# Kernel tuning notes

Hardware: AMD Instinct MI355X
Metric: run time of the kernel (lower is better)

The kernel has to match this reference:

```python
import jax, jax.numpy as jnp
import numpy as np

B, T, C = 4, 2048, 1024
N_HEADS = 16
HEAD_DIM = C // N_HEADS


def setup_inputs() -> dict:
    key = jax.random.key(0)
    k1, k2, k3, k4, k5 = jax.random.split(key, 5)
    x = jax.random.normal(k1, (B, T, C), dtype=jnp.float32)
    # torch Linear: y = x @ W.T + b; store W as [out, in]
    w_qkv = jax.random.normal(k2, (3 * C, C), dtype=jnp.float32) * (1.0 / np.sqrt(C))
    b_qkv = jax.random.normal(k3, (3 * C,), dtype=jnp.float32) * 0.01
    w_proj = jax.random.normal(k4, (C, C), dtype=jnp.float32) * (1.0 / np.sqrt(C))
    b_proj = jax.random.normal(k5, (C,), dtype=jnp.float32) * 0.01
    return {"x": x, "w_qkv": w_qkv, "b_qkv": b_qkv, "w_proj": w_proj, "b_proj": b_proj}


def reference(x, w_qkv, b_qkv, w_proj, b_proj):
    Bx, Tx, Cx = x.shape
    scale = 1.0 / np.sqrt(HEAD_DIM)
    qkv = x @ w_qkv.T + b_qkv                              # [B,T,3C]
    qkv = qkv.reshape(Bx, Tx, 3, N_HEADS, HEAD_DIM)
    qkv = jnp.transpose(qkv, (2, 0, 3, 1, 4))              # [3,B,H,T,D]
    q, k, v = qkv[0], qkv[1], qkv[2]
    att = jnp.einsum('bhqd,bhkd->bhqk', q, k) * scale      # [B,H,T,T]
    causal = jnp.tril(jnp.ones((Tx, Tx), dtype=bool))
    att = jnp.where(causal[None, None, :, :], att, -jnp.inf)
    att = jax.nn.softmax(att, axis=-1)
    # dropout p=0.0 (eval) -> identity
    out = jnp.einsum('bhqk,bhkd->bhqd', att, v)            # [B,H,T,D]
    out = jnp.transpose(out, (0, 2, 1, 3)).reshape(Bx, Tx, Cx)
    return out @ w_proj.T + b_proj
```

## Files before the change

### kernel.cpp

```cpp
#include <hip/hip_runtime.h>
#include <hip/hip_bf16.h>
#include <cstdint>

typedef __attribute__((ext_vector_type(8))) short bf16x8;
typedef __attribute__((ext_vector_type(4))) float f32x4;
typedef __attribute__((ext_vector_type(16))) float f32x16;

#define MFMA16(a, b, c) __builtin_amdgcn_mfma_f32_16x16x32_bf16(a, b, c, 0, 0, 0)
#define MFMA32(a, b, c) __builtin_amdgcn_mfma_f32_32x32x16_bf16(a, b, c, 0, 0, 0)

typedef __attribute__((address_space(1))) uint32_t as1_u32;
typedef __attribute__((address_space(3))) uint32_t as3_u32;
static __device__ __forceinline__ void gload16(const void* g, void* l) {
  __builtin_amdgcn_global_load_lds((as1_u32*)g, (as3_u32*)l, 16, 0, 0);
}

static __device__ __forceinline__ ushort f2b(float f) {
  union { float f; uint32_t u; } v; v.f = f;
  uint32_t u = v.u;
  uint32_t r = (u + 0x7FFFu + ((u >> 16) & 1u)) >> 16;
  return (ushort)r;
}

static __device__ __forceinline__ uint32_t cvtpk(float a, float b) {
  uint32_t r;
  asm("v_cvt_pk_bf16_f32 %0, %1, %2" : "=v"(r) : "v"(a), "v"(b));
  return r;
}
static __device__ __forceinline__ void plswap(uint32_t& a, uint32_t& b) {
  asm volatile("v_permlane32_swap_b32 %0, %1" : "+v"(a), "+v"(b));
}

#define QSCALE 0.1803368782f

#define LOFF(r, kc4) (((r) >> 1) * 64 + ((((((r) & 1) << 2) | (kc4)) ^ (((r) >> 1) & 7)) * 8))

#define N4_X  2097152
#define N4_WQ 786432
#define N4_WP 262144
__global__ void cvt_all(const float* __restrict__ x, const float* __restrict__ wq,
                        const float* __restrict__ wp, ushort* __restrict__ xb,
                        ushort* __restrict__ wqb, ushort* __restrict__ wpb) {
  int i = blockIdx.x * blockDim.x + threadIdx.x;
  const float* src; ushort* dst; int j;
  if (i < N4_X)            { src = x;  dst = xb;  j = i; }
  else if (i < N4_X + N4_WQ) { src = wq; dst = wqb; j = i - N4_X; }
  else                     { src = wp; dst = wpb; j = i - (N4_X + N4_WQ); }
  const float4 v = ((const float4*)src)[j];
  ushort4 o;
  o.x = f2b(v.x); o.y = f2b(v.y); o.z = f2b(v.z); o.w = f2b(v.w);
  ((ushort4*)dst)[j] = o;
}

__global__ __launch_bounds__(512, 2) void gemm_qkv256(
    const ushort* __restrict__ A,
    const ushort* __restrict__ W,
    const float* __restrict__ bias,
    int K, int nbx, int nbase,
    ushort* __restrict__ q_ws, ushort* __restrict__ k_ws, ushort* __restrict__ v_ws) {
  __shared__ ushort As[2][2][2][64 * 64];
  __shared__ ushort Bs[2][2][2][64 * 64];
  const int tid = threadIdx.x;
  const int cpx = gridDim.x >> 3;
  const int wg = (blockIdx.x & 7) * cpx + (blockIdx.x >> 3);
  const int m0 = (wg / nbx) * 256, n0 = nbase + (wg % nbx) * 256;
  const int wid = tid >> 6, lane = tid & 63;
  const int wr = wid >> 2, wc = wid & 3;
  const int lr = lane & 15, lg = lane >> 4;
  const int bhalf = wc >> 1, brow = (wc & 1) * 64;
  const int prow = tid >> 3, pchk = tid & 7;
  const int lchk = pchk ^ (prow & 7);
  const int srow = prow * 2 + (lchk >> 2);
  const int skc = (lchk & 3) * 8;

  f32x4 acc[8][4] = {};
  const int nt = K >> 6;

#define STA(db_, half_, kt_)                                                  \
  { const ushort* src = A + (size_t)(m0 + (half_)*128 + srow) * K + (kt_)*64 + skc; \
    gload16(src, &As[db_][half_][0][tid * 8]);                                \
    gload16(src + 32, &As[db_][half_][1][tid * 8]); }
#define STB(db_, half_, kt_)                                                  \
  { const ushort* src = W + (size_t)(n0 + (half_)*128 + srow) * K + (kt_)*64 + skc; \
    gload16(src, &Bs[db_][half_][0][tid * 8]);                                \
    gload16(src + 32, &Bs[db_][half_][1][tid * 8]); }

  STB(0, 0, 0); STB(0, 1, 0);
  STA(0, 0, 0); STA(0, 1, 0);
  STB(1, 0, 1); STB(1, 1, 1);
  asm volatile("s_waitcnt vmcnt(4)" ::: "memory");
  __builtin_amdgcn_s_barrier();

  for (int T = 0; T < nt; ++T) {
    const int db = T & 1;
    const ushort* Ak0 = &As[db][wr][0][0];
    const ushort* Ak1 = &As[db][wr][1][0];
    const ushort* Bk0 = &Bs[db][bhalf][0][0];
    const ushort* Bk1 = &Bs[db][bhalf][1][0];
    bf16x8 b[4][2];
    {
      bf16x8 a[4][2];
#pragma unroll
      for (int mm = 0; mm < 4; ++mm) {
        const int r = mm * 16 + lr;
        a[mm][0] = *(const bf16x8*)&Ak0[LOFF(r, lg)];
        a[mm][1] = *(const bf16x8*)&Ak1[LOFF(r, lg)];
      }
#pragma unroll
      for (int nf = 0; nf < 4; ++nf) {
        const int rr = brow + nf * 16 + lr;
        b[nf][0] = *(const bf16x8*)&Bk0[LOFF(rr, lg)];
        b[nf][1] = *(const bf16x8*)&Bk1[LOFF(rr, lg)];
      }
      if (T + 1 < nt) { STA(db ^ 1, 0, T + 1); STA(db ^ 1, 1, T + 1); }
      __builtin_amdgcn_sched_barrier(0);
      __builtin_amdgcn_s_barrier();
      asm volatile("s_waitcnt lgkmcnt(0)" ::: "memory");
      __builtin_amdgcn_sched_barrier(0);
      __builtin_amdgcn_s_setprio(1);
#pragma unroll
      for (int kk = 0; kk < 2; ++kk)
#pragma unroll
        for (int mm = 0; mm < 4; ++mm)
#pragma unroll
          for (int nf = 0; nf < 4; ++nf)
            acc[mm][nf] = MFMA16(a[mm][kk], b[nf][kk], acc[mm][nf]);
      __builtin_amdgcn_s_setprio(0);
      __builtin_amdgcn_s_barrier();
    }
    {
      bf16x8 a[4][2];
#pragma unroll
      for (int mm = 0; mm < 4; ++mm) {
        const int r = (4 + mm) * 16 + lr;
        a[mm][0] = *(const bf16x8*)&Ak0[LOFF(r, lg)];
        a[mm][1] = *(const bf16x8*)&Ak1[LOFF(r, lg)];
      }
      if (T + 2 < nt) { STB(db, 0, T + 2); STB(db, 1, T + 2); }
      __builtin_amdgcn_sched_barrier(0);
      __builtin_amdgcn_s_barrier();
      asm volatile("s_waitcnt lgkmcnt(0)" ::: "memory");
      __builtin_amdgcn_sched_barrier(0);
      __builtin_amdgcn_s_setprio(1);
#pragma unroll
      for (int kk = 0; kk < 2; ++kk)
#pragma unroll
        for (int mm = 0; mm < 4; ++mm)
#pragma unroll
          for (int nf = 0; nf < 4; ++nf)
            acc[4 + mm][nf] = MFMA16(a[mm][kk], b[nf][kk], acc[4 + mm][nf]);
      __builtin_amdgcn_s_setprio(0);
      if (T + 2 < nt)
        asm volatile("s_waitcnt vmcnt(4)" ::: "memory");
      else if (T + 1 < nt)
        asm volatile("s_waitcnt vmcnt(0)" ::: "memory");
      if (T + 1 < nt) __builtin_amdgcn_s_barrier();
    }
  }
#undef STA
#undef STB

#pragma unroll
  for (int mf = 0; mf < 8; ++mf) {
#pragma unroll
    for (int nf = 0; nf < 4; ++nf) {
      const int rowb = m0 + wr * 128 + mf * 16 + lg * 4;
      const int col = n0 + wc * 64 + nf * 16 + lr;
      float v[4];
#pragma unroll
      for (int i = 0; i < 4; ++i) v[i] = acc[mf][nf][i] + bias[col];
      const int sel = col >> 10;
      const int rem = col & 1023;
      const int h = rem >> 6, d = rem & 63;
      const int bb = rowb >> 11, t0 = rowb & 2047;
      if (sel == 2) {
        ushort4 st;
        st.x = f2b(v[0]); st.y = f2b(v[1]); st.z = f2b(v[2]); st.w = f2b(v[3]);
        *(ushort4*)&v_ws[((size_t)(bb * 16 + h) * 64 + d) * 2048 + t0] = st;
      } else if (sel == 0) {
#pragma unroll
        for (int i = 0; i < 4; ++i)
          q_ws[((size_t)(bb * 16 + h) * 2048 + t0 + i) * 64 + d] = f2b(v[i] * QSCALE);
      } else {
#pragma unroll
        for (int i = 0; i < 4; ++i)
          k_ws[((size_t)(bb * 16 + h) * 2048 + t0 + i) * 64 + d] = f2b(v[i]);
      }
    }
  }
}

template<int EPI>
__global__ __launch_bounds__(512, 2) void gemm_2ph(
    const ushort* __restrict__ A,
    const ushort* __restrict__ W,
    const float* __restrict__ bias,
    int K, int Nout, int nbx, int nbase,
    ushort* __restrict__ q_ws, ushort* __restrict__ k_ws, ushort* __restrict__ v_ws,
    float* __restrict__ out) {
  __shared__ ushort As[2][2][64 * 64];
  __shared__ ushort Bs[2][2][2][64 * 64];
  const int tid = threadIdx.x;
  const int cpx = gridDim.x >> 3;
  const int wg = (blockIdx.x & 7) * cpx + (blockIdx.x >> 3);
  const int m0 = (wg / nbx) * 128, n0 = nbase + (wg % nbx) * 256;
  const int wid = tid >> 6, lane = tid & 63;
  const int wr = wid >> 2, wc = wid & 3;
  const int lr = lane & 15, lg = lane >> 4;
  const int prow = tid >> 3, pchk = tid & 7;
  const int lchk = pchk ^ (prow & 7);
  const int srow = prow * 2 + (lchk >> 2);
  const int skc = (lchk & 3) * 8;

  f32x4 acc[4][4] = {};
  const int nt = K >> 6;

#define STA(db_, kt_)                                                         \
  { const ushort* src = A + (size_t)(m0 + srow) * K + (kt_)*64 + skc;         \
    gload16(src, &As[db_][0][tid * 8]);                                       \
    gload16(src + 32, &As[db_][1][tid * 8]); }
#define STB(db_, half_, kt_)                                                  \
  { const ushort* src = W + (size_t)(n0 + (half_)*128 + srow) * K + (kt_)*64 + skc; \
    gload16(src, &Bs[db_][half_][0][tid * 8]);                                \
    gload16(src + 32, &Bs[db_][half_][1][tid * 8]); }

  STB(0, 0, 0); STB(0, 1, 0);
  STA(0, 0);
  STB(1, 0, 1); STB(1, 1, 1);
  asm volatile("s_waitcnt vmcnt(4)" ::: "memory");
  __builtin_amdgcn_s_barrier();

  const int bhalf = wc >> 1, brow = (wc & 1) * 64;
  for (int T = 0; T < nt; ++T) {
    const int db = T & 1;
    const ushort* Asub0 = &As[db][0][0];
    const ushort* Asub1 = &As[db][1][0];
    const ushort* Bsub0 = &Bs[db][bhalf][0][0];
    const ushort* Bsub1 = &Bs[db][bhalf][1][0];
    bf16x8 b[4][2];
    {
      bf16x8 a[2][2];
#pragma unroll
      for (int mm = 0; mm < 2; ++mm) {
        const int r = wr * 64 + mm * 16 + lr;
        a[mm][0] = *(const bf16x8*)&Asub0[LOFF(r, lg)];
        a[mm][1] = *(const bf16x8*)&Asub1[LOFF(r, lg)];
      }
#pragma unroll
      for (int nf = 0; nf < 4; ++nf) {
        const int r = brow + nf * 16 + lr;
        b[nf][0] = *(const bf16x8*)&Bsub0[LOFF(r, lg)];
        b[nf][1] = *(const bf16x8*)&Bsub1[LOFF(r, lg)];
      }
      if (T + 1 < nt) STA((T + 1) & 1, T + 1);
      __builtin_amdgcn_sched_barrier(0);
      __builtin_amdgcn_s_barrier();
      asm volatile("s_waitcnt lgkmcnt(0)" ::: "memory");
      __builtin_amdgcn_sched_barrier(0);
      __builtin_amdgcn_s_setprio(1);
#pragma unroll
      for (int kk = 0; kk < 2; ++kk)
#pragma unroll
        for (int mm = 0; mm < 2; ++mm)
#pragma unroll
          for (int nf = 0; nf < 4; ++nf)
            acc[mm][nf] = MFMA16(a[mm][kk], b[nf][kk], acc[mm][nf]);
      __builtin_amdgcn_s_setprio(0);
      __builtin_amdgcn_s_barrier();
    }
    {
      bf16x8 a[2][2];
#pragma unroll
      for (int mm = 0; mm < 2; ++mm) {
        const int r = wr * 64 + (2 + mm) * 16 + lr;
        a[mm][0] = *(const bf16x8*)&Asub0[LOFF(r, lg)];
        a[mm][1] = *(const bf16x8*)&Asub1[LOFF(r, lg)];
      }
      if (T + 2 < nt) { STB(db, 0, T + 2); STB(db, 1, T + 2); }
      __builtin_amdgcn_sched_barrier(0);
      __builtin_amdgcn_s_barrier();
      asm volatile("s_waitcnt lgkmcnt(0)" ::: "memory");
      __builtin_amdgcn_sched_barrier(0);
      __builtin_amdgcn_s_setprio(1);
#pragma unroll
      for (int kk = 0; kk < 2; ++kk)
#pragma unroll
        for (int mm = 0; mm < 2; ++mm)
#pragma unroll
          for (int nf = 0; nf < 4; ++nf)
            acc[2 + mm][nf] = MFMA16(a[mm][kk], b[nf][kk], acc[2 + mm][nf]);
      __builtin_amdgcn_s_setprio(0);
      if (T + 2 < nt)
        asm volatile("s_waitcnt vmcnt(4)" ::: "memory");
      else if (T + 1 < nt)
        asm volatile("s_waitcnt vmcnt(0)" ::: "memory");
      if (T + 1 < nt) __builtin_amdgcn_s_barrier();
    }
  }
#undef STA
#undef STB

#pragma unroll
  for (int mf = 0; mf < 4; ++mf) {
#pragma unroll
    for (int nf = 0; nf < 4; ++nf) {
      const int rowb = m0 + wr * 64 + mf * 16 + lg * 4;
      const int col = n0 + wc * 64 + nf * 16 + lr;
      float v[4];
#pragma unroll
      for (int i = 0; i < 4; ++i) v[i] = acc[mf][nf][i] + bias[col];
      if (EPI == 0) {
        const int sel = col >> 10;
        const int rem = col & 1023;
        const int h = rem >> 6, d = rem & 63;
        const int bb = rowb >> 11, t0 = rowb & 2047;
        if (sel == 2) {
          ushort4 st;
          st.x = f2b(v[0]); st.y = f2b(v[1]); st.z = f2b(v[2]); st.w = f2b(v[3]);
          *(ushort4*)&v_ws[((size_t)(bb * 16 + h) * 64 + d) * 2048 + t0] = st;
        } else if (sel == 0) {
#pragma unroll
          for (int i = 0; i < 4; ++i)
            q_ws[((size_t)(bb * 16 + h) * 2048 + t0 + i) * 64 + d] = f2b(v[i] * QSCALE);
        } else {
#pragma unroll
          for (int i = 0; i < 4; ++i)
            k_ws[((size_t)(bb * 16 + h) * 2048 + t0 + i) * 64 + d] = f2b(v[i]);
        }
      } else {
#pragma unroll
        for (int i = 0; i < 4; ++i)
          out[(size_t)(rowb + i) * Nout + col] = v[i];
      }
    }
  }
}

__global__ __launch_bounds__(256, 4) void attn_v6(
    const ushort* __restrict__ Q, const ushort* __restrict__ K,
    const ushort* __restrict__ VT, ushort* __restrict__ O ) {
  const int blk = blockIdx.x;
  const int s = 15 - (blk >> 6);
  const int bh = blk & 63;
  const int tid = threadIdx.x;
  const int w = tid >> 6, lane = tid & 63;
  const int l31 = lane & 31, l5 = lane >> 5;
  const int bb = bh >> 4, h = bh & 15;
  const size_t base = (size_t)bh * 2048 * 64;
  const ushort* Qb = Q + base;
  const ushort* Kb = K + base;
  const ushort* VTb = VT + base;

  __shared__ ushort Ks[2][64 * 64];
  __shared__ ushort Vs[2][64 * 64];
  __shared__ float l_lds[4][32];

#define STAGE(buf, kt_)                                              \
  do {                                                               \
    const ushort* Kt = Kb + (size_t)(kt_) * 64 * 64;                 \
    const ushort* Vt = VTb + (kt_) * 64;                             \
    _Pragma("unroll") for (int i_ = 0; i_ < 2; ++i_) {               \
      const int ch = i_ * 256 + tid;                                 \
      const int r = ch >> 3;                                         \
      const int csw = ((ch & 7) ^ (r & 7)) * 8;                      \
      gload16(&Kt[(size_t)r * 64 + csw], &Ks[buf][ch * 8]);          \
      gload16(&Vt[(size_t)r * 2048 + csw], &Vs[buf][ch * 8]);        \
    }                                                                \
  } while (0)

  const int q0w = s * 128 + w * 32;
  const int nt = 2 * s + 2;
  const int qlane = q0w + l31;

  bf16x8 qf[4];
#pragma unroll
  for (int dblk = 0; dblk < 4; ++dblk)
    qf[dblk] = *(const bf16x8*)&Qb[(size_t)qlane * 64 + dblk * 16 + l5 * 8];

  f32x16 o0 = {}, o1 = {};
  float lsum = 0.f;

  STAGE(0, 0);
  __syncthreads();

  for (int kt = 0; kt < nt; ++kt) {
    const int cur = kt & 1;
    if (kt + 1 < nt) STAGE(cur ^ 1, kt + 1);
    const int k0 = kt << 6;
    const ushort* Ksc = Ks[cur];
    const ushort* Vsc = Vs[cur];
#pragma unroll
    for (int kblk = 0; kblk < 2; ++kblk) {
      const int kbase = k0 + kblk * 32;
      if (kbase <= q0w + 31) {
        f32x16 st = {};
        __builtin_amdgcn_s_setprio(1);
#pragma unroll
        for (int dblk = 0; dblk < 4; ++dblk) {
          const int row = kblk * 32 + l31;
          bf16x8 ka = *(const bf16x8*)&Ksc[row * 64 + (((dblk * 2 + l5) ^ (row & 7)) * 8)];
          st = MFMA32(ka, qf[dblk], st);
        }
        __builtin_amdgcn_s_setprio(0);
        if (kbase + 31 > q0w) {
#pragma unroll
          for (int r = 0; r < 16; ++r) {
            const int kk = kbase + (r & 3) + 8 * (r >> 2) + 4 * l5;
            st[r] = (kk <= qlane) ? st[r] : -INFINITY;
          }
        }
        float p[16];
#pragma unroll
        for (int r = 0; r < 16; ++r) {
          p[r] = __builtin_amdgcn_exp2f(st[r]);
          lsum += p[r];
        }
#pragma unroll
        for (int sbl = 0; sbl < 2; ++sbl) {
          uint32_t P0 = cvtpk(p[8 * sbl + 0], p[8 * sbl + 1]);
          uint32_t P1 = cvtpk(p[8 * sbl + 2], p[8 * sbl + 3]);
          uint32_t P2 = cvtpk(p[8 * sbl + 4], p[8 * sbl + 5]);
          uint32_t P3 = cvtpk(p[8 * sbl + 6], p[8 * sbl + 7]);
          plswap(P0, P2);
          plswap(P1, P3);
          union { uint32_t u[4]; bf16x8 v; } pk;
          pk.u[0] = P0; pk.u[1] = P1; pk.u[2] = P2; pk.u[3] = P3;
          const int kchunk = kblk * 4 + sbl * 2 + l5;
          __builtin_amdgcn_s_setprio(1);
#pragma unroll
          for (int db2 = 0; db2 < 2; ++db2) {
            const int vrow = db2 * 32 + l31;
            bf16x8 vb = *(const bf16x8*)&Vsc[vrow * 64 + ((kchunk ^ (vrow & 7)) * 8)];
            if (db2 == 0) o0 = MFMA32(pk.v, vb, o0);
            else          o1 = MFMA32(pk.v, vb, o1);
          }
          __builtin_amdgcn_s_setprio(0);
        }
      }
    }
    __syncthreads();
  }

  const float lfull = lsum + __shfl_xor(lsum, 32);
  if (lane < 32) l_lds[w][lane] = 1.f / lfull;
#pragma unroll
  for (int r = 0; r < 16; ++r) {
    const int qoff = (r & 3) + 8 * (r >> 2) + 4 * l5;
    const float inv = l_lds[w][qoff];
    const int t = q0w + qoff;
    ushort* op = &O[(size_t)(bb * 2048 + t) * 1024 + h * 64 + l31];
    op[0] = f2b(o0[r] * inv);
    op[32] = f2b(o1[r] * inv);
  }
#undef STAGE
}

extern "C" void kernel_launch(void* const* d_in, const int* in_sizes, int n_in,
                              void* d_out, int out_size, void* d_ws, size_t ws_size,
                              hipStream_t stream) {
  const float* x = (const float*)d_in[0];
  const float* w_qkv = (const float*)d_in[1];
  const float* b_qkv = (const float*)d_in[2];
  const float* w_proj = (const float*)d_in[3];
  const float* b_proj = (const float*)d_in[4];
  float* out = (float*)d_out;

  char* ws = (char*)d_ws;
  const size_t SZ_X = (size_t)8192 * 1024 * 2;
  const size_t SZ_WQ = (size_t)3072 * 1024 * 2;
  const size_t SZ_WP = (size_t)1024 * 1024 * 2;
  ushort* xb = (ushort*)(ws);
  ushort* wqb = (ushort*)(ws + SZ_X);
  ushort* wpb = (ushort*)(ws + SZ_X + SZ_WQ);
  ushort* q_ws = (ushort*)(ws + SZ_X + SZ_WQ + SZ_WP);
  ushort* k_ws = q_ws + (size_t)8192 * 1024;
  ushort* v_ws = k_ws + (size_t)8192 * 1024;

  cvt_all<<<(N4_X + N4_WQ + N4_WP) / 256, 256, 0, stream>>>(
      x, w_qkv, w_proj, xb, wqb, wpb);

  gemm_qkv256<<<256, 512, 0, stream>>>(
      xb, wqb, b_qkv, 1024, 8, 0, q_ws, k_ws, v_ws);

  gemm_2ph<0><<<256, 512, 0, stream>>>(
      xb, wqb, b_qkv, 1024, 0, 4, 2048, q_ws, k_ws, v_ws, nullptr);

  attn_v6<<<1024, 256, 0, stream>>>(q_ws, k_ws, v_ws, xb);

  gemm_2ph<1><<<256, 512, 0, stream>>>(
      xb, wpb, b_proj, 1024, 1024, 4, 0, nullptr, nullptr, nullptr, out);
}
```

Before: 153.0 us.

## Pipeline attention K/V staging with vmcnt waits and MFMA-based row sums

```diff
diff --git a/kernel.cpp b/kernel.cpp
--- a/kernel.cpp
+++ b/kernel.cpp
@@ -336,7 +336,7 @@
   }
 }
 
-__global__ __launch_bounds__(256, 4) void attn_v6(
+__global__ __launch_bounds__(256, 4) void attn_v7(
     const ushort* __restrict__ Q, const ushort* __restrict__ K,
     const ushort* __restrict__ VT, ushort* __restrict__ O ) {
   const int blk = blockIdx.x;
@@ -353,7 +353,6 @@
 
   __shared__ ushort Ks[2][64 * 64];
   __shared__ ushort Vs[2][64 * 64];
-  __shared__ float l_lds[4][32];
 
 #define STAGE(buf, kt_)                                              \
   do {                                                               \
@@ -372,81 +371,90 @@
   const int nt = 2 * s + 2;
   const int qlane = q0w + l31;
 
+  const int r7 = l31 & 7;
+  int offs[4];
+#pragma unroll
+  for (int i = 0; i < 4; ++i) offs[i] = l31 * 64 + (((2 * i + l5) ^ r7) << 3);
+
   bf16x8 qf[4];
 #pragma unroll
   for (int dblk = 0; dblk < 4; ++dblk)
     qf[dblk] = *(const bf16x8*)&Qb[(size_t)qlane * 64 + dblk * 16 + l5 * 8];
 
-  f32x16 o0 = {}, o1 = {};
-  float lsum = 0.f;
+  const bf16x8 vone = {0x3F80, 0x3F80, 0x3F80, 0x3F80, 0x3F80, 0x3F80, 0x3F80, 0x3F80};
+
+  f32x16 o0 = {}, o1 = {}, lacc = {};
 
   STAGE(0, 0);
-  __syncthreads();
-
-  for (int kt = 0; kt < nt; ++kt) {
-    const int cur = kt & 1;
-    if (kt + 1 < nt) STAGE(cur ^ 1, kt + 1);
-    const int k0 = kt << 6;
-    const ushort* Ksc = Ks[cur];
-    const ushort* Vsc = Vs[cur];
-#pragma unroll
-    for (int kblk = 0; kblk < 2; ++kblk) {
-      const int kbase = k0 + kblk * 32;
-      if (kbase <= q0w + 31) {
-        f32x16 st = {};
-        __builtin_amdgcn_s_setprio(1);
-#pragma unroll
-        for (int dblk = 0; dblk < 4; ++dblk) {
-          const int row = kblk * 32 + l31;
-          bf16x8 ka = *(const bf16x8*)&Ksc[row * 64 + (((dblk * 2 + l5) ^ (row & 7)) * 8)];
-          st = MFMA32(ka, qf[dblk], st);
-        }
-        __builtin_amdgcn_s_setprio(0);
-        if (kbase + 31 > q0w) {
-#pragma unroll
-          for (int r = 0; r < 16; ++r) {
-            const int kk = kbase + (r & 3) + 8 * (r >> 2) + 4 * l5;
-            st[r] = (kk <= qlane) ? st[r] : -INFINITY;
+  asm volatile("s_waitcnt vmcnt(0)" ::: "memory");
+  __builtin_amdgcn_s_barrier();
+
+  for (int kt = 0; kt < nt; kt += 2) {
+#pragma unroll
+    for (int half = 0; half < 2; ++half) {
+      const int t = kt + half;
+      if (t + 1 < nt) {
+        STAGE(half ^ 1, t + 1);
+        asm volatile("s_waitcnt vmcnt(4)" ::: "memory");
+      } else {
+        asm volatile("s_waitcnt vmcnt(0)" ::: "memory");
+      }
+      __builtin_amdgcn_s_barrier();
+
+      const int k0 = t << 6;
+#pragma unroll
+      for (int kblk = 0; kblk < 2; ++kblk) {
+        const int kbase = k0 + kblk * 32;
+        if (kbase <= q0w + 31) {
+          f32x16 st = {};
+          __builtin_amdgcn_s_setprio(1);
+#pragma unroll
+          for (int dblk = 0; dblk < 4; ++dblk) {
+            bf16x8 ka = *(const bf16x8*)&Ks[half][kblk * 2048 + offs[dblk]];
+            st = MFMA32(ka, qf[dblk], st);
+          }
+          __builtin_amdgcn_s_setprio(0);
+          if (kbase + 31 > q0w) {
+#pragma unroll
+            for (int r = 0; r < 16; ++r) {
+              const int kk = kbase + (r & 3) + 8 * (r >> 2) + 4 * l5;
+              st[r] = (kk <= qlane) ? st[r] : -INFINITY;
+            }
+          }
+          float p[16];
+#pragma unroll
+          for (int r = 0; r < 16; ++r) p[r] = __builtin_amdgcn_exp2f(st[r]);
+#pragma unroll
+          for (int sbl = 0; sbl < 2; ++sbl) {
+            uint32_t P0 = cvtpk(p[8 * sbl + 0], p[8 * sbl + 1]);
+            uint32_t P1 = cvtpk(p[8 * sbl + 2], p[8 * sbl + 3]);
+            uint32_t P2 = cvtpk(p[8 * sbl + 4], p[8 * sbl + 5]);
+            uint32_t P3 = cvtpk(p[8 * sbl + 6], p[8 * sbl + 7]);
+            plswap(P0, P2);
+            plswap(P1, P3);
+            union { uint32_t u[4]; bf16x8 v; } pk;
+            pk.u[0] = P0; pk.u[1] = P1; pk.u[2] = P2; pk.u[3] = P3;
+            __builtin_amdgcn_s_setprio(1);
+            lacc = MFMA32(pk.v, vone, lacc);
+#pragma unroll
+            for (int db2 = 0; db2 < 2; ++db2) {
+              bf16x8 vb =
+                  *(const bf16x8*)&Vs[half][db2 * 2048 + offs[kblk * 2 + sbl]];
+              if (db2 == 0) o0 = MFMA32(pk.v, vb, o0);
+              else          o1 = MFMA32(pk.v, vb, o1);
+            }
+            __builtin_amdgcn_s_setprio(0);
           }
         }
-        float p[16];
-#pragma unroll
-        for (int r = 0; r < 16; ++r) {
-          p[r] = __builtin_amdgcn_exp2f(st[r]);
-          lsum += p[r];
-        }
-#pragma unroll
-        for (int sbl = 0; sbl < 2; ++sbl) {
-          uint32_t P0 = cvtpk(p[8 * sbl + 0], p[8 * sbl + 1]);
-          uint32_t P1 = cvtpk(p[8 * sbl + 2], p[8 * sbl + 3]);
-          uint32_t P2 = cvtpk(p[8 * sbl + 4], p[8 * sbl + 5]);
-          uint32_t P3 = cvtpk(p[8 * sbl + 6], p[8 * sbl + 7]);
-          plswap(P0, P2);
-          plswap(P1, P3);
-          union { uint32_t u[4]; bf16x8 v; } pk;
-          pk.u[0] = P0; pk.u[1] = P1; pk.u[2] = P2; pk.u[3] = P3;
-          const int kchunk = kblk * 4 + sbl * 2 + l5;
-          __builtin_amdgcn_s_setprio(1);
-#pragma unroll
-          for (int db2 = 0; db2 < 2; ++db2) {
-            const int vrow = db2 * 32 + l31;
-            bf16x8 vb = *(const bf16x8*)&Vsc[vrow * 64 + ((kchunk ^ (vrow & 7)) * 8)];
-            if (db2 == 0) o0 = MFMA32(pk.v, vb, o0);
-            else          o1 = MFMA32(pk.v, vb, o1);
-          }
-          __builtin_amdgcn_s_setprio(0);
-        }
-      }
-    }
-    __syncthreads();
+      }
+      if (t + 1 < nt) __builtin_amdgcn_s_barrier();
+    }
   }
 
-  const float lfull = lsum + __shfl_xor(lsum, 32);
-  if (lane < 32) l_lds[w][lane] = 1.f / lfull;
 #pragma unroll
   for (int r = 0; r < 16; ++r) {
+    const float inv = 1.f / lacc[r];
     const int qoff = (r & 3) + 8 * (r >> 2) + 4 * l5;
-    const float inv = l_lds[w][qoff];
     const int t = q0w + qoff;
     ushort* op = &O[(size_t)(bb * 2048 + t) * 1024 + h * 64 + l31];
     op[0] = f2b(o0[r] * inv);
@@ -485,7 +493,7 @@
   gemm_2ph<0><<<256, 512, 0, stream>>>(
       xb, wqb, b_qkv, 1024, 0, 4, 2048, q_ws, k_ws, v_ws, nullptr);
 
-  attn_v6<<<1024, 256, 0, stream>>>(q_ws, k_ws, v_ws, xb);
+  attn_v7<<<1024, 256, 0, stream>>>(q_ws, k_ws, v_ws, xb);
 
   gemm_2ph<1><<<256, 512, 0, stream>>>(
       xb, wpb, b_proj, 1024, 1024, 4, 0, nullptr, nullptr, nullptr, out);
```

Result: no change. 153.3 us, median of 2 (+0.2%).
